# Kernel optimization log

Hardware: AMD Instinct MI355X
Metric: run time of the kernel (lower is better)

## Reference

```python
import jax, jax.numpy as jnp
import numpy as np

N = 100000
E = 800000
F_IN = 256
HID = 64
H = 4
NEG_SLOPE = 0.2
BN_EPS = 1e-5


def setup_inputs() -> dict:
    key = jax.random.key(0)
    ks = jax.random.split(key, 20)
    s = 0.05
    return {
        "x": jax.random.normal(ks[0], (N, F_IN), jnp.float32),
        "edge_index": jax.random.randint(ks[1], (2, E), 0, N, jnp.int64),
        # GCNConv params
        "W_gcn": jax.random.normal(ks[2], (F_IN, HID), jnp.float32) * s,
        "b_gcn": jnp.zeros((HID,), jnp.float32),
        "g0": jnp.ones((HID,), jnp.float32),
        "beta0": jnp.zeros((HID,), jnp.float32),
        # GATConv 1 params
        "W1": jax.random.normal(ks[3], (HID, H * HID), jnp.float32) * s,
        "a_src1": jax.random.normal(ks[4], (H, HID), jnp.float32) * s,
        "a_dst1": jax.random.normal(ks[5], (H, HID), jnp.float32) * s,
        "b1": jnp.zeros((H * HID,), jnp.float32),
        "g1": jnp.ones((H * HID,), jnp.float32),
        "beta1": jnp.zeros((H * HID,), jnp.float32),
        # GATConv 2 params
        "W2": jax.random.normal(ks[6], (H * HID, H * HID), jnp.float32) * s,
        "a_src2": jax.random.normal(ks[7], (H, HID), jnp.float32) * s,
        "a_dst2": jax.random.normal(ks[8], (H, HID), jnp.float32) * s,
        "b2": jnp.zeros((H * HID,), jnp.float32),
        "g2": jnp.ones((H * HID,), jnp.float32),
        "beta2": jnp.zeros((H * HID,), jnp.float32),
    }


def _add_self_loops(edge_index, n):
    loop = jnp.arange(n, dtype=edge_index.dtype)
    src = jnp.concatenate([edge_index[0], loop])
    dst = jnp.concatenate([edge_index[1], loop])
    return src, dst


def _batch_norm(x, g, b):
    # BatchNorm1d, training-mode batch stats (biased variance), no dropout
    m = x.mean(0)
    v = x.var(0)
    return g * (x - m) * jax.lax.rsqrt(v + BN_EPS) + b


def _gcn_conv(x, src, dst, W, b, n):
    # symmetric normalization with self-loops already included in src/dst
    deg = jax.ops.segment_sum(jnp.ones_like(dst, jnp.float32), dst, n)
    dinv = jax.lax.rsqrt(jnp.maximum(deg, 1.0))
    norm = dinv[src] * dinv[dst]  # [E']
    h = x @ W  # [N, HID]
    out = jax.ops.segment_sum(h[src] * norm[:, None], dst, n)
    return out + b


def _gat_conv(x, src, dst, W, a_src, a_dst, b, n):
    h = (x @ W).reshape(n, H, HID)  # [N, H, C]
    alpha_s = jnp.einsum("nhc,hc->nh", h, a_src)  # [N, H]
    alpha_d = jnp.einsum("nhc,hc->nh", h, a_dst)
    e = alpha_s[src] + alpha_d[dst]  # [E', H]
    e = jnp.where(e > 0, e, NEG_SLOPE * e)  # LeakyReLU
    # softmax over incoming edges of each dst node, per head
    emax = jax.ops.segment_max(e, dst, n)
    w = jnp.exp(e - emax[dst])
    wsum = jax.ops.segment_sum(w, dst, n)
    att = w / wsum[dst]  # [E', H]
    out = jax.ops.segment_sum(att[:, :, None] * h[src], dst, n)  # [N, H, C]
    return out.reshape(n, H * HID) + b


def reference(x, edge_index, W_gcn, b_gcn, g0, beta0, W1, a_src1, a_dst1, b1,
              g1, beta1, W2, a_src2, a_dst2, b2, g2, beta2):
    n = x.shape[0]
    src, dst = _add_self_loops(edge_index, n)
    h = jax.nn.relu(_gcn_conv(x, src, dst, W_gcn, b_gcn, n))
    h = _batch_norm(h, g0, beta0)
    h = _gat_conv(h, src, dst, W1, a_src1, a_dst1, b1, n)
    h = jax.nn.elu(_batch_norm(h, g1, beta1))
    h = _gat_conv(h, src, dst, W2, a_src2, a_dst2, b2, n)
    h = jax.nn.elu(_batch_norm(h, g2, beta2))
    return h
```

## Files before the change

### kernel.cpp

```cpp
#include <hip/hip_runtime.h>
#include <hip/hip_bf16.h>
#include <math.h>

#define NN 100000
#define EE 800000
#define FIN 256
#define CH 64
#define C1 256
#define BN_EPS 1e-5f
#define NEG_SLOPE 0.2f

typedef __attribute__((ext_vector_type(8))) short short8;
typedef __attribute__((ext_vector_type(8))) unsigned short u16x8;
typedef __attribute__((ext_vector_type(4))) float f32x4;

__device__ __forceinline__ float bf2f(ushort u) {
    return __uint_as_float(((unsigned)u) << 16);
}
__device__ __forceinline__ ushort f2bf(float f) {
    unsigned u = __float_as_uint(f);
    return (ushort)((u + 0x7FFF + ((u >> 16) & 1)) >> 16);
}

__global__ void hist_kernel(const int* __restrict__ ei, int* __restrict__ deg) {
    int t = blockIdx.x * 256 + threadIdx.x;
    if (t < EE) atomicAdd(&deg[ei[EE + t]], 1);
}
__global__ void scan_k1(const int* __restrict__ deg, int* __restrict__ row_start,
                        int* __restrict__ bsum, float* __restrict__ dinv) {
    __shared__ int sh[256];
    int t = threadIdx.x;
    int i = blockIdx.x * 256 + t;
    int v = (i < NN) ? (deg[i] + 1) : 0;
    if (i < NN) dinv[i] = rsqrtf((float)v);
    sh[t] = v;
    __syncthreads();
    for (int off = 1; off < 256; off <<= 1) {
        int add = (t >= off) ? sh[t - off] : 0;
        __syncthreads();
        sh[t] += add;
        __syncthreads();
    }
    if (i < NN) row_start[i] = sh[t] - v;
    if (t == 255) bsum[blockIdx.x] = sh[255];
}
__global__ void scan_k2(int* __restrict__ bsum, int nb) {
    __shared__ int sh[512];
    int t = threadIdx.x;
    int v = (t < nb) ? bsum[t] : 0;
    sh[t] = v;
    __syncthreads();
    for (int off = 1; off < 512; off <<= 1) {
        int add = (t >= off) ? sh[t - off] : 0;
        __syncthreads();
        sh[t] += add;
        __syncthreads();
    }
    if (t < nb) bsum[t] = sh[t] - v;
}
__global__ void scan_k3(int* __restrict__ row_start, const int* __restrict__ bsum) {
    int i = blockIdx.x * 256 + threadIdx.x;
    if (i < NN) row_start[i] += bsum[i >> 8];
    if (i == NN) row_start[NN] = EE + NN;
}
__global__ void scatter_kernel(const int* __restrict__ ei, const int* __restrict__ row_start,
                               int* __restrict__ fill, int* __restrict__ sorted) {
    int t = blockIdx.x * 256 + threadIdx.x;
    if (t >= EE + NN) return;
    int s, d;
    if (t < EE) { s = ei[t]; d = ei[EE + t]; }
    else        { s = t - EE; d = s; }
    int pos = atomicAdd(&fill[d], 1);
    sorted[row_start[d] + pos] = s;
}

__global__ void transpose_all(const float* __restrict__ Wg, const float* __restrict__ W1,
                              const float* __restrict__ W2, ushort* __restrict__ Wgt,
                              ushort* __restrict__ W1t, ushort* __restrict__ W2t) {
    int idx = blockIdx.x * 256 + threadIdx.x;
    if (idx < FIN * CH) {
        int m = idx / CH, n = idx % CH;
        Wgt[n * FIN + m] = f2bf(Wg[idx]);
    } else if (idx < FIN * CH + CH * C1) {
        int i = idx - FIN * CH;
        int m = i / C1, n = i % C1;
        W1t[n * CH + m] = f2bf(W1[i]);
    } else if (idx < FIN * CH + CH * C1 + C1 * C1) {
        int i = idx - FIN * CH - CH * C1;
        int m = i / C1, n = i % C1;
        W2t[n * C1 + m] = f2bf(W2[i]);
    }
}

template<int AMODE>
__global__ __launch_bounds__(256) void gemm_mfma(
        const void* __restrict__ Ap, const ushort* __restrict__ Bt,
        ushort* __restrict__ C, int M, int K,
        const float* __restrict__ t_bias, const float* __restrict__ t_scale,
        const float* __restrict__ t_shift,
        const float* __restrict__ a_src, const float* __restrict__ a_dst,
        float* __restrict__ alpha_s, float* __restrict__ alpha_d) {
    __shared__ ushort As[64][40];
    __shared__ ushort Bs[64][40];
    int t = threadIdx.x;
    int w = t >> 6;
    int l = t & 63;
    int rowBase = blockIdx.y * 64;
    int colBase = blockIdx.x * 64;
    int srow = t >> 2;
    int sk = (t & 3) * 8;
    int m = l & 15, q = l >> 4;
    f32x4 acc[4] = {};
    for (int k0 = 0; k0 < M; k0 += 32) {
        int gr = rowBase + srow;
        int ch = k0 + sk;
        ushort4 u0 = {0, 0, 0, 0}, u1 = {0, 0, 0, 0};
        if (AMODE == 1) {
            if (gr < NN) {
                const float* Af = (const float*)Ap;
                float4 f0 = *(const float4*)&Af[(long)gr * M + ch];
                float4 f1 = *(const float4*)&Af[(long)gr * M + ch + 4];
                u0.x = f2bf(f0.x); u0.y = f2bf(f0.y); u0.z = f2bf(f0.z); u0.w = f2bf(f0.w);
                u1.x = f2bf(f1.x); u1.y = f2bf(f1.y); u1.z = f2bf(f1.z); u1.w = f2bf(f1.w);
            }
        } else if (AMODE == 2) {
            if (gr < NN) {
                const float* Af = (const float*)Ap;
                float4 f0 = *(const float4*)&Af[(long)gr * M + ch];
                float4 f1 = *(const float4*)&Af[(long)gr * M + ch + 4];
                f32x4 b0 = *(const f32x4*)&t_bias[ch],  b1 = *(const f32x4*)&t_bias[ch + 4];
                f32x4 s0 = *(const f32x4*)&t_scale[ch], s1 = *(const f32x4*)&t_scale[ch + 4];
                f32x4 h0 = *(const f32x4*)&t_shift[ch], h1 = *(const f32x4*)&t_shift[ch + 4];
                u0.x = f2bf(s0[0] * fmaxf(f0.x + b0[0], 0.f) + h0[0]);
                u0.y = f2bf(s0[1] * fmaxf(f0.y + b0[1], 0.f) + h0[1]);
                u0.z = f2bf(s0[2] * fmaxf(f0.z + b0[2], 0.f) + h0[2]);
                u0.w = f2bf(s0[3] * fmaxf(f0.w + b0[3], 0.f) + h0[3]);
                u1.x = f2bf(s1[0] * fmaxf(f1.x + b1[0], 0.f) + h1[0]);
                u1.y = f2bf(s1[1] * fmaxf(f1.y + b1[1], 0.f) + h1[1]);
                u1.z = f2bf(s1[2] * fmaxf(f1.z + b1[2], 0.f) + h1[2]);
                u1.w = f2bf(s1[3] * fmaxf(f1.w + b1[3], 0.f) + h1[3]);
            }
        } else {
            if (gr < NN) {
                const ushort* Ab = (const ushort*)Ap;
                u16x8 y = *(const u16x8*)&Ab[(long)gr * M + ch];
                f32x4 s0 = *(const f32x4*)&t_scale[ch], s1 = *(const f32x4*)&t_scale[ch + 4];
                f32x4 h0 = *(const f32x4*)&t_shift[ch], h1 = *(const f32x4*)&t_shift[ch + 4];
                float r[8];
#pragma unroll
                for (int j = 0; j < 8; ++j) {
                    float sc = (j < 4) ? s0[j] : s1[j - 4];
                    float sh = (j < 4) ? h0[j] : h1[j - 4];
                    float v = sc * bf2f((ushort)y[j]) + sh;
                    r[j] = (v > 0.f) ? v : (__expf(v) - 1.f);
                }
                u0.x = f2bf(r[0]); u0.y = f2bf(r[1]); u0.z = f2bf(r[2]); u0.w = f2bf(r[3]);
                u1.x = f2bf(r[4]); u1.y = f2bf(r[5]); u1.z = f2bf(r[6]); u1.w = f2bf(r[7]);
            }
        }
        *(ushort4*)&As[srow][sk] = u0;
        *(ushort4*)&As[srow][sk + 4] = u1;
        uint4 bv = *(const uint4*)&Bt[(long)(colBase + srow) * M + k0 + sk];
        *(uint4*)&Bs[srow][sk] = bv;
        __syncthreads();
        short8 af = *(const short8*)&As[w * 16 + m][q * 8];
#pragma unroll
        for (int c = 0; c < 4; ++c) {
            short8 bf = *(const short8*)&Bs[c * 16 + m][q * 8];
            acc[c] = __builtin_amdgcn_mfma_f32_16x16x32_bf16(af, bf, acc[c], 0, 0, 0);
        }
        __syncthreads();
    }
    if (alpha_s) {
        int head = colBase >> 6;
        float ps[4] = {}, pd[4] = {};
#pragma unroll
        for (int c = 0; c < 4; ++c) {
            float av = a_src[colBase + c * 16 + m];
            float dv = a_dst[colBase + c * 16 + m];
#pragma unroll
            for (int r = 0; r < 4; ++r) {
                ps[r] += acc[c][r] * av;
                pd[r] += acc[c][r] * dv;
            }
        }
#pragma unroll
        for (int r = 0; r < 4; ++r) {
            ps[r] += __shfl_xor(ps[r], 1); pd[r] += __shfl_xor(pd[r], 1);
            ps[r] += __shfl_xor(ps[r], 2); pd[r] += __shfl_xor(pd[r], 2);
            ps[r] += __shfl_xor(ps[r], 4); pd[r] += __shfl_xor(pd[r], 4);
            ps[r] += __shfl_xor(ps[r], 8); pd[r] += __shfl_xor(pd[r], 8);
        }
        if (m == 0) {
#pragma unroll
            for (int r = 0; r < 4; ++r) {
                int row = rowBase + w * 16 + q * 4 + r;
                if (row < NN) {
                    alpha_s[row * 4 + head] = ps[r];
                    alpha_d[row * 4 + head] = pd[r];
                }
            }
        }
    }
#pragma unroll
    for (int c = 0; c < 4; ++c) {
#pragma unroll
        for (int r = 0; r < 4; ++r) {
            int orow = rowBase + w * 16 + q * 4 + r;
            if (orow < NN) C[(long)orow * K + colBase + c * 16 + m] = f2bf(acc[c][r]);
        }
    }
}

__global__ __launch_bounds__(256) void gcn_gather(
        const int* __restrict__ row_start, const int* __restrict__ sorted,
        const float* __restrict__ dinv, const ushort* __restrict__ h0,
        float* __restrict__ agg) {
    int node = blockIdx.x * 4 + (threadIdx.x >> 6);
    if (node >= NN) return;
    int l = threadIdx.x & 63;
    int slot = l >> 3;
    int li = l & 7;
    int c = li * 8;
    int b = row_start[node], e = row_start[node + 1];
    float a[8] = {};
    for (int i = b + slot; i < e; i += 8) {
        int s = sorted[i];
        float dv = dinv[s];
        u16x8 v = *(const u16x8*)&h0[(long)s * 64 + c];
#pragma unroll
        for (int j = 0; j < 8; ++j) a[j] += dv * bf2f((ushort)v[j]);
    }
#pragma unroll
    for (int j = 0; j < 8; ++j) {
        a[j] += __shfl_xor(a[j], 8);
        a[j] += __shfl_xor(a[j], 16);
        a[j] += __shfl_xor(a[j], 32);
    }
    if (slot == 0) {
        float dn = dinv[node];
        f32x4 o0, o1;
#pragma unroll
        for (int j = 0; j < 4; ++j) { o0[j] = a[j] * dn; o1[j] = a[4 + j] * dn; }
        *(f32x4*)&agg[(long)node * 64 + c] = o0;
        *(f32x4*)&agg[(long)node * 64 + c + 4] = o1;
    }
}

__global__ __launch_bounds__(256) void bn_stats64(
        const float* __restrict__ x, const float* __restrict__ bias,
        float* __restrict__ sums, float* __restrict__ sumsq) {
    __shared__ float red[4][16][8];
    int l = threadIdx.x & 63;
    int w = threadIdx.x >> 6;
    int wv = blockIdx.x * 4 + w;
    int nw = gridDim.x * 4;
    int sub = l >> 4;
    int c = (l & 15) * 4;
    f32x4 b4 = *(const f32x4*)&bias[c];
    float s0 = 0.f, s1 = 0.f, s2 = 0.f, s3 = 0.f;
    float q0 = 0.f, q1 = 0.f, q2 = 0.f, q3 = 0.f;
    for (int r = wv * 4 + sub; r < NN; r += nw * 4) {
        f32x4 v = *(const f32x4*)&x[(long)r * 64 + c];
        float v0 = fmaxf(v[0] + b4[0], 0.f);
        float v1 = fmaxf(v[1] + b4[1], 0.f);
        float v2 = fmaxf(v[2] + b4[2], 0.f);
        float v3 = fmaxf(v[3] + b4[3], 0.f);
        s0 += v0; s1 += v1; s2 += v2; s3 += v3;
        q0 += v0 * v0; q1 += v1 * v1; q2 += v2 * v2; q3 += v3 * v3;
    }
    s0 += __shfl_xor(s0, 16); s1 += __shfl_xor(s1, 16);
    s2 += __shfl_xor(s2, 16); s3 += __shfl_xor(s3, 16);
    q0 += __shfl_xor(q0, 16); q1 += __shfl_xor(q1, 16);
    q2 += __shfl_xor(q2, 16); q3 += __shfl_xor(q3, 16);
    s0 += __shfl_xor(s0, 32); s1 += __shfl_xor(s1, 32);
    s2 += __shfl_xor(s2, 32); s3 += __shfl_xor(s3, 32);
    q0 += __shfl_xor(q0, 32); q1 += __shfl_xor(q1, 32);
    q2 += __shfl_xor(q2, 32); q3 += __shfl_xor(q3, 32);
    if (sub == 0) {
        int li = l & 15;
        red[w][li][0] = s0; red[w][li][1] = s1; red[w][li][2] = s2; red[w][li][3] = s3;
        red[w][li][4] = q0; red[w][li][5] = q1; red[w][li][6] = q2; red[w][li][7] = q3;
    }
    __syncthreads();
    if (w == 0 && sub == 0) {
        int li = l & 15;
        atomicAdd(&sums[c + 0], red[0][li][0] + red[1][li][0] + red[2][li][0] + red[3][li][0]);
        atomicAdd(&sums[c + 1], red[0][li][1] + red[1][li][1] + red[2][li][1] + red[3][li][1]);
        atomicAdd(&sums[c + 2], red[0][li][2] + red[1][li][2] + red[2][li][2] + red[3][li][2]);
        atomicAdd(&sums[c + 3], red[0][li][3] + red[1][li][3] + red[2][li][3] + red[3][li][3]);
        atomicAdd(&sumsq[c + 0], red[0][li][4] + red[1][li][4] + red[2][li][4] + red[3][li][4]);
        atomicAdd(&sumsq[c + 1], red[0][li][5] + red[1][li][5] + red[2][li][5] + red[3][li][5]);
        atomicAdd(&sumsq[c + 2], red[0][li][6] + red[1][li][6] + red[2][li][6] + red[3][li][6]);
        atomicAdd(&sumsq[c + 3], red[0][li][7] + red[1][li][7] + red[2][li][7] + red[3][li][7]);
    }
}
__global__ __launch_bounds__(256) void bn_stats256(
        const ushort* __restrict__ x,
        float* __restrict__ sums, float* __restrict__ sumsq) {
    __shared__ float red[4][64][8];
    int l = threadIdx.x & 63;
    int w = threadIdx.x >> 6;
    int wv = blockIdx.x * 4 + w;
    int nw = gridDim.x * 4;
    int c = l * 4;
    float s0 = 0.f, s1 = 0.f, s2 = 0.f, s3 = 0.f;
    float q0 = 0.f, q1 = 0.f, q2 = 0.f, q3 = 0.f;
    for (int r = wv; r < NN; r += nw) {
        ushort4 v = *(const ushort4*)&x[(long)r * 256 + c];
        float v0 = bf2f(v.x), v1 = bf2f(v.y), v2 = bf2f(v.z), v3 = bf2f(v.w);
        s0 += v0; s1 += v1; s2 += v2; s3 += v3;
        q0 += v0 * v0; q1 += v1 * v1; q2 += v2 * v2; q3 += v3 * v3;
    }
    red[w][l][0] = s0; red[w][l][1] = s1; red[w][l][2] = s2; red[w][l][3] = s3;
    red[w][l][4] = q0; red[w][l][5] = q1; red[w][l][6] = q2; red[w][l][7] = q3;
    __syncthreads();
    if (w == 0) {
        atomicAdd(&sums[c + 0], red[0][l][0] + red[1][l][0] + red[2][l][0] + red[3][l][0]);
        atomicAdd(&sums[c + 1], red[0][l][1] + red[1][l][1] + red[2][l][1] + red[3][l][1]);
        atomicAdd(&sums[c + 2], red[0][l][2] + red[1][l][2] + red[2][l][2] + red[3][l][2]);
        atomicAdd(&sums[c + 3], red[0][l][3] + red[1][l][3] + red[2][l][3] + red[3][l][3]);
        atomicAdd(&sumsq[c + 0], red[0][l][4] + red[1][l][4] + red[2][l][4] + red[3][l][4]);
        atomicAdd(&sumsq[c + 1], red[0][l][5] + red[1][l][5] + red[2][l][5] + red[3][l][5]);
        atomicAdd(&sumsq[c + 2], red[0][l][6] + red[1][l][6] + red[2][l][6] + red[3][l][6]);
        atomicAdd(&sumsq[c + 3], red[0][l][7] + red[1][l][7] + red[2][l][7] + red[3][l][7]);
    }
}
__global__ void bn_finalize(const float* __restrict__ sums, const float* __restrict__ sumsq,
                            const float* __restrict__ g, const float* __restrict__ beta,
                            float* __restrict__ scale, float* __restrict__ shift, int C) {
    int c = threadIdx.x;
    if (c < C) {
        float mean = sums[c] / (float)NN;
        float var = sumsq[c] / (float)NN - mean * mean;
        float sc = g[c] * rsqrtf(var + BN_EPS);
        scale[c] = sc;
        shift[c] = beta[c] - mean * sc;
    }
}
__global__ __launch_bounds__(256) void bn_apply_gat(
        const ushort* __restrict__ x,
        const float* __restrict__ scale, const float* __restrict__ shift,
        float* __restrict__ out) {
    int l = threadIdx.x & 63;
    int wv = blockIdx.x * 4 + (threadIdx.x >> 6);
    int nw = gridDim.x * 4;
    int c = l * 4;
    f32x4 sc4 = *(const f32x4*)&scale[c];
    f32x4 sh4 = *(const f32x4*)&shift[c];
    for (int r = wv; r < NN; r += nw) {
        ushort4 v = *(const ushort4*)&x[(long)r * 256 + c];
        float t0 = sc4[0] * bf2f(v.x) + sh4[0];
        float t1 = sc4[1] * bf2f(v.y) + sh4[1];
        float t2 = sc4[2] * bf2f(v.z) + sh4[2];
        float t3 = sc4[3] * bf2f(v.w) + sh4[3];
        f32x4 o;
        o[0] = (t0 > 0.f) ? t0 : (__expf(t0) - 1.f);
        o[1] = (t1 > 0.f) ? t1 : (__expf(t1) - 1.f);
        o[2] = (t2 > 0.f) ? t2 : (__expf(t2) - 1.f);
        o[3] = (t3 > 0.f) ? t3 : (__expf(t3) - 1.f);
        *(f32x4*)&out[(long)r * 256 + c] = o;
    }
}

__global__ __launch_bounds__(256) void gat_gather(
        const int* __restrict__ row_start, const int* __restrict__ sorted,
        const float* __restrict__ as, const float* __restrict__ ad,
        const ushort* __restrict__ h, ushort* __restrict__ out) {
    int node = blockIdx.x * 4 + (threadIdx.x >> 6);
    if (node >= NN) return;
    int l = threadIdx.x & 63;
    int head = l >> 4;
    int b = row_start[node], e = row_start[node + 1];
    float adn = ad[node * 4 + head];
    float a0 = 0.f, a1 = 0.f, a2 = 0.f, a3 = 0.f;
    float ls = 0.f;
    int i = b;
    for (; i + 3 < e; i += 4) {
        int s[4]; float ev[4]; ushort4 v[4];
#pragma unroll
        for (int j = 0; j < 4; ++j) s[j] = sorted[i + j];
#pragma unroll
        for (int j = 0; j < 4; ++j) ev[j] = as[s[j] * 4 + head];
#pragma unroll
        for (int j = 0; j < 4; ++j) v[j] = *(const ushort4*)&h[(long)s[j] * 256 + l * 4];
#pragma unroll
        for (int j = 0; j < 4; ++j) {
            float t = ev[j] + adn;
            t = (t > 0.f) ? t : NEG_SLOPE * t;
            float wt = __expf(t);
            ls += wt;
            a0 += wt * bf2f(v[j].x);
            a1 += wt * bf2f(v[j].y);
            a2 += wt * bf2f(v[j].z);
            a3 += wt * bf2f(v[j].w);
        }
    }
    for (; i < e; ++i) {
        int sv = sorted[i];
        float t = as[sv * 4 + head] + adn;
        t = (t > 0.f) ? t : NEG_SLOPE * t;
        float wt = __expf(t);
        ushort4 v0 = *(const ushort4*)&h[(long)sv * 256 + l * 4];
        ls += wt;
        a0 += wt * bf2f(v0.x);
        a1 += wt * bf2f(v0.y);
        a2 += wt * bf2f(v0.z);
        a3 += wt * bf2f(v0.w);
    }
    float inv = 1.0f / ls;
    ushort4 o;
    o.x = f2bf(a0 * inv);
    o.y = f2bf(a1 * inv);
    o.z = f2bf(a2 * inv);
    o.w = f2bf(a3 * inv);
    *(ushort4*)&out[(long)node * 256 + l * 4] = o;
}

extern "C" void kernel_launch(void* const* d_in, const int* in_sizes, int n_in,
                              void* d_out, int out_size, void* d_ws, size_t ws_size,
                              hipStream_t stream) {
    const float* x      = (const float*)d_in[0];
    const int*   ei     = (const int*)d_in[1];
    const float* W_gcn  = (const float*)d_in[2];
    const float* b_gcn  = (const float*)d_in[3];
    const float* g0     = (const float*)d_in[4];
    const float* beta0  = (const float*)d_in[5];
    const float* W1     = (const float*)d_in[6];
    const float* a_src1 = (const float*)d_in[7];
    const float* a_dst1 = (const float*)d_in[8];
    const float* b1     = (const float*)d_in[9];
    const float* g1     = (const float*)d_in[10];
    const float* beta1  = (const float*)d_in[11];
    const float* W2     = (const float*)d_in[12];
    const float* a_src2 = (const float*)d_in[13];
    const float* a_dst2 = (const float*)d_in[14];
    const float* b2     = (const float*)d_in[15];
    const float* g2     = (const float*)d_in[16];
    const float* beta2  = (const float*)d_in[17];

    const long N = NN;
    float* ws = (float*)d_ws;

    float* dinv    = ws;
    float* alpha_s = ws + N;
    float* alpha_d = ws + 5 * N;
    float* sums0   = ws + 9 * N;
    float* sumsq0  = sums0 + 64;
    float* sums1   = sumsq0 + 64;
    float* sumsq1  = sums1 + 256;
    float* sums2   = sumsq1 + 256;
    float* sumsq2  = sums2 + 256;
    float* scale   = sumsq2 + 256;
    float* shift   = scale + 256;
    int*   row_start = (int*)(shift + 256);
    int*   fill      = row_start + NN + 1;
    int*   deg_i     = fill + NN;
    int*   sorted    = deg_i + NN;
    int*   bsum      = sorted + EE + NN;
    ushort* Wgt  = (ushort*)(ws + 23 * N);
    ushort* W1t  = Wgt + 16384;
    ushort* W2t  = W1t + 16384;
    ushort* h0b  = (ushort*)(ws + 24 * N);
    float*  agg0 = ws + 56 * N;
    ushort* h1b  = (ushort*)(ws + 120 * N);
    ushort* yb   = (ushort*)(ws + 376 * N);
    float*  outp = (float*)d_out;

    const int BLK = 256;
    dim3 blk(BLK);
    const int NBLK_N = (NN + 255) / 256;

    hipMemsetAsync(fill, 0, 2L * NN * sizeof(int), stream);
    hipMemsetAsync(sums0, 0, 1152 * sizeof(float), stream);
    hist_kernel<<<(EE + 255) / 256, blk, 0, stream>>>(ei, deg_i);
    scan_k1<<<NBLK_N, blk, 0, stream>>>(deg_i, row_start, bsum, dinv);
    scan_k2<<<1, 512, 0, stream>>>(bsum, NBLK_N);
    scan_k3<<<(NN + 1 + 255) / 256, blk, 0, stream>>>(row_start, bsum);
    scatter_kernel<<<(EE + NN + 255) / 256, blk, 0, stream>>>(ei, row_start, fill, sorted);

    transpose_all<<<(FIN * CH + CH * C1 + C1 * C1 + 255) / 256, blk, 0, stream>>>(
        W_gcn, W1, W2, Wgt, W1t, W2t);

    gemm_mfma<1><<<dim3(CH / 64, (NN + 63) / 64), blk, 0, stream>>>(
        x, Wgt, h0b, FIN, CH, nullptr, nullptr, nullptr,
        nullptr, nullptr, nullptr, nullptr);
    gcn_gather<<<(NN + 3) / 4, blk, 0, stream>>>(row_start, sorted, dinv, h0b, agg0);
    bn_stats64<<<512, blk, 0, stream>>>(agg0, b_gcn, sums0, sumsq0);
    bn_finalize<<<1, CH, 0, stream>>>(sums0, sumsq0, g0, beta0, scale, shift, CH);

    gemm_mfma<2><<<dim3(C1 / 64, (NN + 63) / 64), blk, 0, stream>>>(
        agg0, W1t, h1b, CH, C1, b_gcn, scale, shift,
        a_src1, a_dst1, alpha_s, alpha_d);
    gat_gather<<<(NN + 3) / 4, blk, 0, stream>>>(row_start, sorted, alpha_s, alpha_d, h1b, yb);
    bn_stats256<<<512, blk, 0, stream>>>(yb, sums1, sumsq1);
    bn_finalize<<<1, C1, 0, stream>>>(sums1, sumsq1, g1, beta1, scale, shift, C1);

    gemm_mfma<3><<<dim3(C1 / 64, (NN + 63) / 64), blk, 0, stream>>>(
        yb, W2t, h1b, C1, C1, nullptr, scale, shift,
        a_src2, a_dst2, alpha_s, alpha_d);
    gat_gather<<<(NN + 3) / 4, blk, 0, stream>>>(row_start, sorted, alpha_s, alpha_d, h1b, yb);
    bn_stats256<<<512, blk, 0, stream>>>(yb, sums2, sumsq2);
    bn_finalize<<<1, C1, 0, stream>>>(sums2, sumsq2, g2, beta2, scale, shift, C1);
    bn_apply_gat<<<2048, blk, 0, stream>>>(yb, scale, shift, outp);
}
```

Measured before the change: 792.1 us.

## Compute all output columns per GEMM block to reuse transformed A tiles

```diff
diff --git a/kernel.cpp b/kernel.cpp
--- a/kernel.cpp
+++ b/kernel.cpp
@@ -92,7 +92,7 @@
     }
 }
 
-template<int AMODE>
+template<int AMODE, int NCOLB>
 __global__ __launch_bounds__(256) void gemm_mfma(
         const void* __restrict__ Ap, const ushort* __restrict__ Bt,
         ushort* __restrict__ C, int M, int K,
@@ -101,16 +101,16 @@
         const float* __restrict__ a_src, const float* __restrict__ a_dst,
         float* __restrict__ alpha_s, float* __restrict__ alpha_d) {
     __shared__ ushort As[64][40];
-    __shared__ ushort Bs[64][40];
+    __shared__ ushort Bs[64 * NCOLB][40];
     int t = threadIdx.x;
     int w = t >> 6;
     int l = t & 63;
     int rowBase = blockIdx.y * 64;
-    int colBase = blockIdx.x * 64;
+    int colBase = blockIdx.x * 64 * NCOLB;
     int srow = t >> 2;
     int sk = (t & 3) * 8;
     int m = l & 15, q = l >> 4;
-    f32x4 acc[4] = {};
+    f32x4 acc[4 * NCOLB] = {};
     for (int k0 = 0; k0 < M; k0 += 32) {
         int gr = rowBase + srow;
         int ch = k0 + sk;
@@ -160,54 +160,63 @@
         }
         *(ushort4*)&As[srow][sk] = u0;
         *(ushort4*)&As[srow][sk + 4] = u1;
-        uint4 bv = *(const uint4*)&Bt[(long)(colBase + srow) * M + k0 + sk];
-        *(uint4*)&Bs[srow][sk] = bv;
+#pragma unroll
+        for (int cb = 0; cb < NCOLB; ++cb) {
+            uint4 bv = *(const uint4*)&Bt[(long)(colBase + cb * 64 + srow) * M + k0 + sk];
+            *(uint4*)&Bs[cb * 64 + srow][sk] = bv;
+        }
         __syncthreads();
         short8 af = *(const short8*)&As[w * 16 + m][q * 8];
 #pragma unroll
-        for (int c = 0; c < 4; ++c) {
-            short8 bf = *(const short8*)&Bs[c * 16 + m][q * 8];
-            acc[c] = __builtin_amdgcn_mfma_f32_16x16x32_bf16(af, bf, acc[c], 0, 0, 0);
+        for (int cf = 0; cf < 4 * NCOLB; ++cf) {
+            short8 bf = *(const short8*)&Bs[cf * 16 + m][q * 8];
+            acc[cf] = __builtin_amdgcn_mfma_f32_16x16x32_bf16(af, bf, acc[cf], 0, 0, 0);
         }
         __syncthreads();
     }
     if (alpha_s) {
-        int head = colBase >> 6;
-        float ps[4] = {}, pd[4] = {};
-#pragma unroll
-        for (int c = 0; c < 4; ++c) {
-            float av = a_src[colBase + c * 16 + m];
-            float dv = a_dst[colBase + c * 16 + m];
+        float ps[4][4] = {}, pd[4][4] = {};
+#pragma unroll
+        for (int cf = 0; cf < 4 * NCOLB; ++cf) {
+            int hh = cf >> 2;
+            float av = a_src[colBase + cf * 16 + m];
+            float dv = a_dst[colBase + cf * 16 + m];
 #pragma unroll
             for (int r = 0; r < 4; ++r) {
-                ps[r] += acc[c][r] * av;
-                pd[r] += acc[c][r] * dv;
+                ps[hh][r] += acc[cf][r] * av;
+                pd[hh][r] += acc[cf][r] * dv;
             }
         }
 #pragma unroll
-        for (int r = 0; r < 4; ++r) {
-            ps[r] += __shfl_xor(ps[r], 1); pd[r] += __shfl_xor(pd[r], 1);
-            ps[r] += __shfl_xor(ps[r], 2); pd[r] += __shfl_xor(pd[r], 2);
-            ps[r] += __shfl_xor(ps[r], 4); pd[r] += __shfl_xor(pd[r], 4);
-            ps[r] += __shfl_xor(ps[r], 8); pd[r] += __shfl_xor(pd[r], 8);
+        for (int hh = 0; hh < 4; ++hh) {
+#pragma unroll
+            for (int r = 0; r < 4; ++r) {
+                ps[hh][r] += __shfl_xor(ps[hh][r], 1); pd[hh][r] += __shfl_xor(pd[hh][r], 1);
+                ps[hh][r] += __shfl_xor(ps[hh][r], 2); pd[hh][r] += __shfl_xor(pd[hh][r], 2);
+                ps[hh][r] += __shfl_xor(ps[hh][r], 4); pd[hh][r] += __shfl_xor(pd[hh][r], 4);
+                ps[hh][r] += __shfl_xor(ps[hh][r], 8); pd[hh][r] += __shfl_xor(pd[hh][r], 8);
+            }
         }
         if (m == 0) {
 #pragma unroll
             for (int r = 0; r < 4; ++r) {
                 int row = rowBase + w * 16 + q * 4 + r;
                 if (row < NN) {
-                    alpha_s[row * 4 + head] = ps[r];
-                    alpha_d[row * 4 + head] = pd[r];
+#pragma unroll
+                    for (int hh = 0; hh < 4; ++hh) {
+                        alpha_s[row * 4 + hh] = ps[hh][r];
+                        alpha_d[row * 4 + hh] = pd[hh][r];
+                    }
                 }
             }
         }
     }
 #pragma unroll
-    for (int c = 0; c < 4; ++c) {
+    for (int cf = 0; cf < 4 * NCOLB; ++cf) {
 #pragma unroll
         for (int r = 0; r < 4; ++r) {
             int orow = rowBase + w * 16 + q * 4 + r;
-            if (orow < NN) C[(long)orow * K + colBase + c * 16 + m] = f2bf(acc[c][r]);
+            if (orow < NN) C[(long)orow * K + colBase + cf * 16 + m] = f2bf(acc[cf][r]);
         }
     }
 }
@@ -482,21 +491,21 @@
     transpose_all<<<(FIN * CH + CH * C1 + C1 * C1 + 255) / 256, blk, 0, stream>>>(
         W_gcn, W1, W2, Wgt, W1t, W2t);
 
-    gemm_mfma<1><<<dim3(CH / 64, (NN + 63) / 64), blk, 0, stream>>>(
+    gemm_mfma<1, 1><<<dim3(1, (NN + 63) / 64), blk, 0, stream>>>(
         x, Wgt, h0b, FIN, CH, nullptr, nullptr, nullptr,
         nullptr, nullptr, nullptr, nullptr);
     gcn_gather<<<(NN + 3) / 4, blk, 0, stream>>>(row_start, sorted, dinv, h0b, agg0);
     bn_stats64<<<512, blk, 0, stream>>>(agg0, b_gcn, sums0, sumsq0);
     bn_finalize<<<1, CH, 0, stream>>>(sums0, sumsq0, g0, beta0, scale, shift, CH);
 
-    gemm_mfma<2><<<dim3(C1 / 64, (NN + 63) / 64), blk, 0, stream>>>(
+    gemm_mfma<2, 4><<<dim3(1, (NN + 63) / 64), blk, 0, stream>>>(
         agg0, W1t, h1b, CH, C1, b_gcn, scale, shift,
         a_src1, a_dst1, alpha_s, alpha_d);
     gat_gather<<<(NN + 3) / 4, blk, 0, stream>>>(row_start, sorted, alpha_s, alpha_d, h1b, yb);
     bn_stats256<<<512, blk, 0, stream>>>(yb, sums1, sumsq1);
     bn_finalize<<<1, C1, 0, stream>>>(sums1, sumsq1, g1, beta1, scale, shift, C1);
 
-    gemm_mfma<3><<<dim3(C1 / 64, (NN + 63) / 64), blk, 0, stream>>>(
+    gemm_mfma<3, 4><<<dim3(1, (NN + 63) / 64), blk, 0, stream>>>(
         yb, W2t, h1b, C1, C1, nullptr, scale, shift,
         a_src2, a_dst2, alpha_s, alpha_d);
     gat_gather<<<(NN + 3) / 4, blk, 0, stream>>>(row_start, sorted, alpha_s, alpha_d, h1b, yb);
```

New measurement: 823.4 us. 1.04x slower.
